# Kernel tuning notes

Hardware: AMD Instinct MI355X
Metric: run time of the kernel (lower is better)

The kernel has to match this reference:

```python
import jax, jax.numpy as jnp
import numpy as np

EPS = 1e-8
THRESHOLD_FACTOR = 0.5


def setup_inputs() -> dict:
    key = jax.random.key(0)
    k1, k2, k3 = jax.random.split(key, 3)
    B, S, D_IN, D_OUT = 4, 4096, 2048, 2048
    x = jax.random.normal(k1, (B, S, D_IN), dtype=jnp.float32)
    # kaiming-uniform-like init for weight
    bound = 1.0 / np.sqrt(D_IN)
    weight = jax.random.uniform(k2, (D_OUT, D_IN), dtype=jnp.float32,
                                minval=-np.sqrt(3.0) * bound, maxval=np.sqrt(3.0) * bound)
    row_scale = jnp.ones((D_OUT, 1), dtype=jnp.float32)
    bias = jax.random.uniform(k3, (D_OUT,), dtype=jnp.float32, minval=-bound, maxval=bound)
    g = jnp.ones((D_IN,), dtype=jnp.float32)  # input RMSNorm affine weight
    return {"x": x, "weight": weight, "row_scale": row_scale, "bias": bias, "g": g}


def _rms_norm(v, axis):
    return v * jax.lax.rsqrt(jnp.mean(v * v, axis=axis, keepdims=True) + EPS)


def reference(x, weight, row_scale, bias, g):
    # input RMSNorm with affine scale
    xn = _rms_norm(x, -1) * g  # [B,S,Din]
    # row RMSNorm of weight
    w = _rms_norm(weight, 1)  # [Dout,Din]
    # abs-mean threshold ternary quantization
    abs_mean = jnp.mean(jnp.abs(w), axis=1, keepdims=True)  # [Dout,1]
    mask = (jnp.abs(w) > THRESHOLD_FACTOR * abs_mean).astype(w.dtype)
    w_q = jnp.sign(w) * mask  # ternary {-1,0,1}
    # scaled dequant: per-row abs_mean and learned row_scale
    w_eff = w_q * abs_mean * row_scale  # [Dout,Din]
    out = jnp.einsum('bsd,od->bso', xn, w_eff) + bias
    return out
```

## Files before the change

### kernel.cpp

```cpp
#include <hip/hip_runtime.h>
#include <stdint.h>

#define EPSF 1e-8f

using i32x4 = __attribute__((ext_vector_type(4))) int;

__device__ __forceinline__ float wave_sum(float v) {
#pragma unroll
  for (int off = 32; off > 0; off >>= 1) v += __shfl_down(v, off, 64);
  return v;
}
__device__ __forceinline__ float wave_max(float v) {
#pragma unroll
  for (int off = 32; off > 0; off >>= 1) v = fmaxf(v, __shfl_down(v, off, 64));
  return v;
}

__global__ __launch_bounds__(256) void wquant_kernel(
    const float* __restrict__ w, const float* __restrict__ row_scale,
    signed char* __restrict__ wq, float* __restrict__ scale, int K) {
  const int row = blockIdx.x;
  const int t = threadIdx.x;
  const float* wr = w + (size_t)row * K;
  float4 v0 = reinterpret_cast<const float4*>(wr)[2 * t];
  float4 v1 = reinterpret_cast<const float4*>(wr)[2 * t + 1];
  float f[8] = {v0.x, v0.y, v0.z, v0.w, v1.x, v1.y, v1.z, v1.w};
  float sa = 0.f, sq = 0.f;
#pragma unroll
  for (int i = 0; i < 8; ++i) { sa += fabsf(f[i]); sq += f[i] * f[i]; }
  sa = wave_sum(sa);
  sq = wave_sum(sq);
  __shared__ float smA[4], smQ[4];
  const int wid = t >> 6;
  if ((t & 63) == 0) { smA[wid] = sa; smQ[wid] = sq; }
  __syncthreads();
  const float sumabs = smA[0] + smA[1] + smA[2] + smA[3];
  const float sumsq  = smQ[0] + smQ[1] + smQ[2] + smQ[3];
  const float absmean = sumabs / (float)K;
  const float thr = 0.5f * absmean;
  union { signed char c[8]; uint2 u; } pk;
#pragma unroll
  for (int i = 0; i < 8; ++i)
    pk.c[i] = (fabsf(f[i]) > thr) ? (f[i] > 0.f ? (signed char)1 : (signed char)-1)
                                  : (signed char)0;
  reinterpret_cast<uint2*>(wq + (size_t)row * K)[t] = pk.u;
  if (t == 0)
    scale[row] = absmean * rsqrtf(sumsq / (float)K + EPSF) * row_scale[row];
}

__global__ __launch_bounds__(256) void xnorm_kernel(
    const float* __restrict__ x, const float* __restrict__ g,
    signed char* __restrict__ xq, float* __restrict__ sx, int K) {
  const int row = blockIdx.x;
  const int t = threadIdx.x;
  const float* xr = x + (size_t)row * K;
  float4 v0 = reinterpret_cast<const float4*>(xr)[2 * t];
  float4 v1 = reinterpret_cast<const float4*>(xr)[2 * t + 1];
  float f[8] = {v0.x, v0.y, v0.z, v0.w, v1.x, v1.y, v1.z, v1.w};
  float sq = 0.f;
#pragma unroll
  for (int i = 0; i < 8; ++i) sq += f[i] * f[i];
  sq = wave_sum(sq);
  __shared__ float smQ[4], smM[4];
  const int wid = t >> 6;
  if ((t & 63) == 0) smQ[wid] = sq;
  __syncthreads();
  const float sumsq = smQ[0] + smQ[1] + smQ[2] + smQ[3];
  const float rs = rsqrtf(sumsq / (float)K + EPSF);
  float4 g0 = reinterpret_cast<const float4*>(g)[2 * t];
  float4 g1 = reinterpret_cast<const float4*>(g)[2 * t + 1];
  float gg[8] = {g0.x, g0.y, g0.z, g0.w, g1.x, g1.y, g1.z, g1.w};
  float vv[8]; float am = 0.f;
#pragma unroll
  for (int i = 0; i < 8; ++i) {
    vv[i] = f[i] * rs * gg[i];
    am = fmaxf(am, fabsf(vv[i]));
  }
  am = wave_max(am);
  if ((t & 63) == 0) smM[wid] = am;
  __syncthreads();
  const float amax = fmaxf(fmaxf(smM[0], smM[1]), fmaxf(smM[2], smM[3]));
  const float inv = amax > 0.f ? 127.f / amax : 0.f;
  union { signed char c[8]; uint2 u; } pk;
#pragma unroll
  for (int i = 0; i < 8; ++i)
    pk.c[i] = (signed char)__float2int_rn(vv[i] * inv);
  reinterpret_cast<uint2*>(xq + (size_t)row * K)[t] = pk.u;
  if (t == 0) sx[row] = amax > 0.f ? amax / 127.f : 0.f;
}


#define BAR() do { __builtin_amdgcn_sched_barrier(0); \
                   asm volatile("" ::: "memory"); \
                   __builtin_amdgcn_s_barrier(); \
                   asm volatile("" ::: "memory"); \
                   __builtin_amdgcn_sched_barrier(0); } while (0)
#define VM(n) asm volatile("s_waitcnt vmcnt(" #n ")" ::: "memory")

__global__ __launch_bounds__(512, 2) void gemm_kernel(
    const signed char* __restrict__ A,
    const signed char* __restrict__ B,
    const float* __restrict__ scale, const float* __restrict__ bias,
    const float* __restrict__ sx,
    float* __restrict__ C, int M, int N, int K) {
  __shared__ signed char lds[2][2][2][16384];

  const int tid  = threadIdx.x;
  const int lane = tid & 63;
  const int wid  = tid >> 6;
  const int wm   = wid >> 2;
  const int wn   = wid & 3;
  const int fr   = lane & 15;
  const int kq   = lane >> 4;

  const int nwg = gridDim.x;
  const int cpx = nwg >> 3;
  const int swz = (blockIdx.x & 7) * cpx + (blockIdx.x >> 3);
  const int NBN = N >> 8;
  const int bn = swz % NBN;
  const int bm = swz / NBN;
  const int mBase = bm * 256, nBase = bn * 256;

  const size_t Kb = (size_t)K;

  const int sr = tid >> 3;
  const int gsrc = (tid & 7) ^ (sr & 7);
  const char* Abyte = (const char*)A + (size_t)(mBase + sr) * Kb + gsrc * 16;
  const char* Bbyte = (const char*)B +
      (size_t)(nBase + ((sr >> 5) * 64) + (sr & 31)) * Kb + gsrc * 16;

#define STAGE_A(bufi, h, t) do { \
    __builtin_amdgcn_global_load_lds( \
      (const __attribute__((address_space(1))) void*)(Abyte + (size_t)((h) * 64) * Kb + (size_t)(t) * 128), \
      (__attribute__((address_space(3))) void*)(&lds[bufi][0][h][tid * 16]), 16, 0, 0); \
    __builtin_amdgcn_global_load_lds( \
      (const __attribute__((address_space(1))) void*)(Abyte + (size_t)(128 + (h) * 64) * Kb + (size_t)(t) * 128), \
      (__attribute__((address_space(3))) void*)(&lds[bufi][0][h][8192 + tid * 16]), 16, 0, 0); \
  } while (0)

#define STAGE_B(bufi, h, t) do { \
    __builtin_amdgcn_global_load_lds( \
      (const __attribute__((address_space(1))) void*)(Bbyte + (size_t)((h) * 32) * Kb + (size_t)(t) * 128), \
      (__attribute__((address_space(3))) void*)(&lds[bufi][1][h][tid * 16]), 16, 0, 0); \
    __builtin_amdgcn_global_load_lds( \
      (const __attribute__((address_space(1))) void*)(Bbyte + (size_t)(128 + (h) * 32) * Kb + (size_t)(t) * 128), \
      (__attribute__((address_space(3))) void*)(&lds[bufi][1][h][8192 + tid * 16]), 16, 0, 0); \
  } while (0)

  const int slot0 = ((kq ^ (fr & 7)) << 4);
  const int aRowB = (wm * 64 + fr) * 128;
  const int bRowB = (wn * 32 + fr) * 128;

  i32x4 aF[4][2], bF[4][2];
  i32x4 acc[8][4];
#pragma unroll
  for (int m = 0; m < 8; ++m)
#pragma unroll
    for (int n = 0; n < 4; ++n) acc[m][n] = (i32x4){0, 0, 0, 0};

#define LDA(bufi, mg) do { \
    _Pragma("unroll") for (int mm = 0; mm < 4; ++mm) \
    _Pragma("unroll") for (int s = 0; s < 2; ++s) \
      aF[mm][s] = *(const i32x4*)&lds[bufi][0][mg][ \
          aRowB + mm * 2048 + (slot0 ^ (s << 6))]; \
  } while (0)

#define LDB(bufi, np) do { \
    _Pragma("unroll") for (int nn = 0; nn < 2; ++nn) \
    _Pragma("unroll") for (int s = 0; s < 2; ++s) \
      bF[(np) * 2 + nn][s] = *(const i32x4*)&lds[bufi][1][np][ \
          bRowB + nn * 2048 + (slot0 ^ (s << 6))]; \
  } while (0)

#define MFMA_Q(mg, np) do { \
    __builtin_amdgcn_s_setprio(1); \
    _Pragma("unroll") for (int mm = 0; mm < 4; ++mm) \
    _Pragma("unroll") for (int nn = 0; nn < 2; ++nn) { \
      i32x4 c = acc[(mg) * 4 + mm][(np) * 2 + nn]; \
      c = __builtin_amdgcn_mfma_i32_16x16x64_i8(aF[mm][0], bF[(np) * 2 + nn][0], c, 0, 0, 0); \
      c = __builtin_amdgcn_mfma_i32_16x16x64_i8(aF[mm][1], bF[(np) * 2 + nn][1], c, 0, 0, 0); \
      acc[(mg) * 4 + mm][(np) * 2 + nn] = c; \
    } \
    __builtin_amdgcn_s_setprio(0); } while (0)

  const int crowBase = mBase + wm * 128 + kq * 4;
  const int ccolBase = nBase + wn * 64 + fr;

#define STORE_Q(mg, np) do { \
    float sxq_[4][4]; \
    _Pragma("unroll") for (int mm = 0; mm < 4; ++mm) \
    _Pragma("unroll") for (int r = 0; r < 4; ++r) \
      sxq_[mm][r] = sx[crowBase + ((mg) * 4 + mm) * 16 + r]; \
    _Pragma("unroll") for (int nn = 0; nn < 2; ++nn) { \
      const int gc = ccolBase + ((np) * 2 + nn) * 16; \
      const float sc = scale[gc]; \
      const float bi = bias[gc]; \
      _Pragma("unroll") for (int mm = 0; mm < 4; ++mm) { \
        const int r0 = crowBase + ((mg) * 4 + mm) * 16; \
        _Pragma("unroll") for (int r = 0; r < 4; ++r) \
          C[(size_t)(r0 + r) * (size_t)N + (size_t)gc] = \
              (float)acc[(mg) * 4 + mm][(np) * 2 + nn][r] * (sxq_[mm][r] * sc) + bi; \
      } } } while (0)

  STAGE_A(0, 0, 0); STAGE_B(0, 0, 0);
  STAGE_A(0, 1, 0); STAGE_B(0, 1, 0);
  STAGE_A(1, 0, 1); STAGE_B(1, 0, 1);
  VM(8);
  BAR();

  const int NT = K >> 7;
  for (int i = 0; i < (NT >> 1) - 1; ++i) {
    const int t1  = 2 * i + 1;
    const int tn0 = 2 * i + 2;
    const int tn1 = 2 * i + 3;
    LDA(0, 0); LDB(0, 0); STAGE_A(1, 1, t1); VM(6);
    BAR(); MFMA_Q(0, 0);
    LDB(0, 1); STAGE_B(1, 1, t1);
    BAR(); MFMA_Q(0, 1);
    LDA(0, 1); STAGE_A(0, 0, tn0);
    BAR(); MFMA_Q(1, 0);
    STAGE_B(0, 0, tn0); VM(8);
    BAR(); MFMA_Q(1, 1);
    LDA(1, 0); LDB(1, 0); STAGE_A(0, 1, tn0); VM(6);
    BAR(); MFMA_Q(0, 0);
    LDB(1, 1); STAGE_B(0, 1, tn0);
    BAR(); MFMA_Q(0, 1);
    LDA(1, 1); STAGE_A(1, 0, tn1);
    BAR(); MFMA_Q(1, 0);
    STAGE_B(1, 0, tn1); VM(8);
    BAR(); MFMA_Q(1, 1);
  }

  {
    const int tl = NT - 1;
    LDA(0, 0); LDB(0, 0); STAGE_A(1, 1, tl); VM(6);
    BAR(); MFMA_Q(0, 0);
    LDB(0, 1); STAGE_B(1, 1, tl);
    BAR(); MFMA_Q(0, 1);
    LDA(0, 1);
    BAR(); MFMA_Q(1, 0);
    VM(4);
    BAR(); MFMA_Q(1, 1);
    LDA(1, 0); LDB(1, 0); VM(0);
    BAR(); MFMA_Q(0, 0); STORE_Q(0, 0);
    LDB(1, 1);
    BAR(); MFMA_Q(0, 1); STORE_Q(0, 1);
    LDA(1, 1);
    BAR(); MFMA_Q(1, 0); STORE_Q(1, 0);
    BAR(); MFMA_Q(1, 1); STORE_Q(1, 1);
  }
#undef STAGE_A
#undef STAGE_B
#undef LDA
#undef LDB
#undef MFMA_Q
#undef STORE_Q
}

extern "C" void kernel_launch(void* const* d_in, const int* in_sizes, int n_in,
                              void* d_out, int out_size, void* d_ws, size_t ws_size,
                              hipStream_t stream) {
  const float* x         = (const float*)d_in[0];
  const float* weight    = (const float*)d_in[1];
  const float* row_scale = (const float*)d_in[2];
  const float* bias      = (const float*)d_in[3];
  const float* g         = (const float*)d_in[4];
  float* out = (float*)d_out;

  const int Din  = in_sizes[4];
  const int Dout = in_sizes[3];
  const int Mrows = in_sizes[0] / Din;

  char* ws = (char*)d_ws;
  signed char* wq = (signed char*)ws;
  signed char* xq = (signed char*)(ws + (size_t)Dout * Din);
  float* scale = (float*)(ws + (size_t)Dout * Din + (size_t)Mrows * Din);
  float* sx = scale + Dout;

  wquant_kernel<<<Dout, 256, 0, stream>>>(weight, row_scale, wq, scale, Din);
  xnorm_kernel<<<Mrows, 256, 0, stream>>>(x, g, xq, sx, Din);
  const int grid = (Mrows / 256) * (Dout / 256);
  gemm_kernel<<<grid, 512, 0, stream>>>(xq, wq, scale, bias, sx, out,
                                        Mrows, Dout, Din);
}
```

Baseline: 114.2 us.

## Switch int8 GEMM inner product to 32x32x32 MFMA tiles

Replaces the 16x16x64 int8 MFMA with the 32x32x32 variant. The LDS fragment loads, accumulator layout and epilogue row/column mapping are reworked to match the new lane layout. Larger MFMA tiles carry more work per instruction and reuse each operand fragment more, which should lower LDS read traffic and instruction-issue overhead. The cost is a new swizzle and store mapping that must line up with the existing staging layout, and strided epilogue writes.

```diff
diff --git a/kernel.cpp b/kernel.cpp
--- a/kernel.cpp
+++ b/kernel.cpp
@@ -3,7 +3,8 @@
 
 #define EPSF 1e-8f
 
-using i32x4 = __attribute__((ext_vector_type(4))) int;
+using i32x4  = __attribute__((ext_vector_type(4))) int;
+using i32x16 = __attribute__((ext_vector_type(16))) int;
 
 __device__ __forceinline__ float wave_sum(float v) {
 #pragma unroll
@@ -110,8 +111,8 @@
   const int wid  = tid >> 6;
   const int wm   = wid >> 2;
   const int wn   = wid & 3;
-  const int fr   = lane & 15;
-  const int kq   = lane >> 4;
+  const int l31  = lane & 31;
+  const int b5   = lane >> 5;
 
   const int nwg = gridDim.x;
   const int cpx = nwg >> 3;
@@ -147,59 +148,56 @@
       (__attribute__((address_space(3))) void*)(&lds[bufi][1][h][8192 + tid * 16]), 16, 0, 0); \
   } while (0)
 
-  const int slot0 = ((kq ^ (fr & 7)) << 4);
-  const int aRowB = (wm * 64 + fr) * 128;
-  const int bRowB = (wn * 32 + fr) * 128;
-
-  i32x4 aF[4][2], bF[4][2];
-  i32x4 acc[8][4];
-#pragma unroll
-  for (int m = 0; m < 8; ++m)
-#pragma unroll
-    for (int n = 0; n < 4; ++n) acc[m][n] = (i32x4){0, 0, 0, 0};
+  const int slotB0 = ((b5 ^ (lane & 7)) << 4);
+  const int aRowB = (wm * 64 + l31) * 128;
+  const int bRowB = (wn * 32 + l31) * 128;
+
+  i32x4 aF[2][4], bF[2][4];
+  i32x16 acc[4][2];
+#pragma unroll
+  for (int m = 0; m < 4; ++m)
+#pragma unroll
+    for (int n = 0; n < 2; ++n)
+#pragma unroll
+      for (int r = 0; r < 16; ++r) acc[m][n][r] = 0;
 
 #define LDA(bufi, mg) do { \
-    _Pragma("unroll") for (int mm = 0; mm < 4; ++mm) \
-    _Pragma("unroll") for (int s = 0; s < 2; ++s) \
-      aF[mm][s] = *(const i32x4*)&lds[bufi][0][mg][ \
-          aRowB + mm * 2048 + (slot0 ^ (s << 6))]; \
+    _Pragma("unroll") for (int mt2 = 0; mt2 < 2; ++mt2) \
+    _Pragma("unroll") for (int s = 0; s < 4; ++s) \
+      aF[mt2][s] = *(const i32x4*)&lds[bufi][0][mg][ \
+          aRowB + mt2 * 4096 + (slotB0 ^ (s << 5))]; \
   } while (0)
 
 #define LDB(bufi, np) do { \
-    _Pragma("unroll") for (int nn = 0; nn < 2; ++nn) \
-    _Pragma("unroll") for (int s = 0; s < 2; ++s) \
-      bF[(np) * 2 + nn][s] = *(const i32x4*)&lds[bufi][1][np][ \
-          bRowB + nn * 2048 + (slot0 ^ (s << 6))]; \
+    _Pragma("unroll") for (int s = 0; s < 4; ++s) \
+      bF[np][s] = *(const i32x4*)&lds[bufi][1][np][ \
+          bRowB + (slotB0 ^ (s << 5))]; \
   } while (0)
 
 #define MFMA_Q(mg, np) do { \
     __builtin_amdgcn_s_setprio(1); \
-    _Pragma("unroll") for (int mm = 0; mm < 4; ++mm) \
-    _Pragma("unroll") for (int nn = 0; nn < 2; ++nn) { \
-      i32x4 c = acc[(mg) * 4 + mm][(np) * 2 + nn]; \
-      c = __builtin_amdgcn_mfma_i32_16x16x64_i8(aF[mm][0], bF[(np) * 2 + nn][0], c, 0, 0, 0); \
-      c = __builtin_amdgcn_mfma_i32_16x16x64_i8(aF[mm][1], bF[(np) * 2 + nn][1], c, 0, 0, 0); \
-      acc[(mg) * 4 + mm][(np) * 2 + nn] = c; \
-    } \
+    _Pragma("unroll") for (int s = 0; s < 4; ++s) \
+    _Pragma("unroll") for (int mt2 = 0; mt2 < 2; ++mt2) \
+      acc[(mg) * 2 + mt2][np] = __builtin_amdgcn_mfma_i32_32x32x32_i8( \
+          aF[mt2][s], bF[np][s], acc[(mg) * 2 + mt2][np], 0, 0, 0); \
     __builtin_amdgcn_s_setprio(0); } while (0)
 
-  const int crowBase = mBase + wm * 128 + kq * 4;
-  const int ccolBase = nBase + wn * 64 + fr;
+  const int crow32 = mBase + wm * 128 + 4 * b5;
+  const int ccol32 = nBase + wn * 64 + l31;
 
 #define STORE_Q(mg, np) do { \
-    float sxq_[4][4]; \
-    _Pragma("unroll") for (int mm = 0; mm < 4; ++mm) \
-    _Pragma("unroll") for (int r = 0; r < 4; ++r) \
-      sxq_[mm][r] = sx[crowBase + ((mg) * 4 + mm) * 16 + r]; \
-    _Pragma("unroll") for (int nn = 0; nn < 2; ++nn) { \
-      const int gc = ccolBase + ((np) * 2 + nn) * 16; \
-      const float sc = scale[gc]; \
-      const float bi = bias[gc]; \
-      _Pragma("unroll") for (int mm = 0; mm < 4; ++mm) { \
-        const int r0 = crowBase + ((mg) * 4 + mm) * 16; \
-        _Pragma("unroll") for (int r = 0; r < 4; ++r) \
-          C[(size_t)(r0 + r) * (size_t)N + (size_t)gc] = \
-              (float)acc[(mg) * 4 + mm][(np) * 2 + nn][r] * (sxq_[mm][r] * sc) + bi; \
+    const int gc = ccol32 + (np) * 32; \
+    const float sc = scale[gc]; \
+    const float bi = bias[gc]; \
+    _Pragma("unroll") for (int mt2 = 0; mt2 < 2; ++mt2) { \
+      const int rb = crow32 + (mg) * 64 + mt2 * 32; \
+      float sxv[16]; \
+      _Pragma("unroll") for (int reg = 0; reg < 16; ++reg) \
+        sxv[reg] = sx[rb + (reg & 3) + 8 * (reg >> 2)]; \
+      _Pragma("unroll") for (int reg = 0; reg < 16; ++reg) { \
+        const int r = rb + (reg & 3) + 8 * (reg >> 2); \
+        C[(size_t)r * (size_t)N + (size_t)gc] = \
+            (float)acc[(mg) * 2 + mt2][np][reg] * (sxv[reg] * sc) + bi; \
       } } } while (0)
 
   STAGE_A(0, 0, 0); STAGE_B(0, 0, 0);
```

Result: slower. 124.1 us (+8.7%).

## Halve barriers per K-tile pair by regrouping staging, LDS reads and MFMAs

Applied to the files above, without the earlier changes.

Reorders the GEMM main loop so each half-tile has two barriers instead of four, issuing both A and B global-to-LDS stages together and grouping MFMA quadrants in pairs. The aim is to cut barrier stalls and the vmcnt waits between MFMA groups. In exchange, each MFMA burst waits longer on LDS reads and there is a risk of LDS buffer hazards if stage/read ordering is wrong.

```diff
diff --git a/kernel.cpp b/kernel.cpp
--- a/kernel.cpp
+++ b/kernel.cpp
@@ -205,49 +205,47 @@
   STAGE_A(0, 0, 0); STAGE_B(0, 0, 0);
   STAGE_A(0, 1, 0); STAGE_B(0, 1, 0);
   STAGE_A(1, 0, 1); STAGE_B(1, 0, 1);
-  VM(8);
-  BAR();
 
   const int NT = K >> 7;
   for (int i = 0; i < (NT >> 1) - 1; ++i) {
     const int t1  = 2 * i + 1;
     const int tn0 = 2 * i + 2;
     const int tn1 = 2 * i + 3;
-    LDA(0, 0); LDB(0, 0); STAGE_A(1, 1, t1); VM(6);
-    BAR(); MFMA_Q(0, 0);
-    LDB(0, 1); STAGE_B(1, 1, t1);
-    BAR(); MFMA_Q(0, 1);
-    LDA(0, 1); STAGE_A(0, 0, tn0);
-    BAR(); MFMA_Q(1, 0);
-    STAGE_B(0, 0, tn0); VM(8);
-    BAR(); MFMA_Q(1, 1);
-    LDA(1, 0); LDB(1, 0); STAGE_A(0, 1, tn0); VM(6);
-    BAR(); MFMA_Q(0, 0);
-    LDB(1, 1); STAGE_B(0, 1, tn0);
-    BAR(); MFMA_Q(0, 1);
-    LDA(1, 1); STAGE_A(1, 0, tn1);
-    BAR(); MFMA_Q(1, 0);
-    STAGE_B(1, 0, tn1); VM(8);
-    BAR(); MFMA_Q(1, 1);
+    VM(4); BAR();
+    STAGE_A(1, 1, t1); STAGE_B(1, 1, t1);
+    LDA(0, 0); LDB(0, 0); LDB(0, 1);
+    MFMA_Q(0, 0); MFMA_Q(0, 1);
+    BAR();
+    STAGE_A(0, 0, tn0); STAGE_B(0, 0, tn0);
+    LDA(0, 1);
+    MFMA_Q(1, 0); MFMA_Q(1, 1);
+    VM(4); BAR();
+    STAGE_A(0, 1, tn0); STAGE_B(0, 1, tn0);
+    LDA(1, 0); LDB(1, 0); LDB(1, 1);
+    MFMA_Q(0, 0); MFMA_Q(0, 1);
+    BAR();
+    STAGE_A(1, 0, tn1); STAGE_B(1, 0, tn1);
+    LDA(1, 1);
+    MFMA_Q(1, 0); MFMA_Q(1, 1);
   }
 
   {
     const int tl = NT - 1;
-    LDA(0, 0); LDB(0, 0); STAGE_A(1, 1, tl); VM(6);
-    BAR(); MFMA_Q(0, 0);
-    LDB(0, 1); STAGE_B(1, 1, tl);
-    BAR(); MFMA_Q(0, 1);
+    VM(4); BAR();
+    STAGE_A(1, 1, tl); STAGE_B(1, 1, tl);
+    LDA(0, 0); LDB(0, 0); LDB(0, 1);
+    MFMA_Q(0, 0); MFMA_Q(0, 1);
+    BAR();
     LDA(0, 1);
-    BAR(); MFMA_Q(1, 0);
-    VM(4);
-    BAR(); MFMA_Q(1, 1);
-    LDA(1, 0); LDB(1, 0); VM(0);
-    BAR(); MFMA_Q(0, 0); STORE_Q(0, 0);
-    LDB(1, 1);
-    BAR(); MFMA_Q(0, 1); STORE_Q(0, 1);
+    MFMA_Q(1, 0); MFMA_Q(1, 1);
+    VM(0); BAR();
+    LDA(1, 0); LDB(1, 0); LDB(1, 1);
+    MFMA_Q(0, 0); STORE_Q(0, 0);
+    MFMA_Q(0, 1); STORE_Q(0, 1);
+    BAR();
     LDA(1, 1);
-    BAR(); MFMA_Q(1, 0); STORE_Q(1, 0);
-    BAR(); MFMA_Q(1, 1); STORE_Q(1, 1);
+    MFMA_Q(1, 0); STORE_Q(1, 0);
+    MFMA_Q(1, 1); STORE_Q(1, 1);
   }
 #undef STAGE_A
 #undef STAGE_B
```

New measurement: 116.4 us. No clear change (+1.9%).

## Fuse prep kernels and compute two N tiles per GEMM block

Applied to the files above, without the earlier changes.

The weight-quantize and activation-normalize kernels are merged into one launch, with blocks split by index, to drop a launch and let both kinds of row work share the device. The GEMM block now computes two adjacent 256-column output tiles in sequence, reusing the A rows. It also prefetches the second tile's operands while the first tile's epilogue stores run. This halves the GEMM grid to one block per CU, which may reduce latency hiding compared with two co-resident blocks per CU.

```diff
diff --git a/kernel.cpp b/kernel.cpp
--- a/kernel.cpp
+++ b/kernel.cpp
@@ -16,77 +16,76 @@
   return v;
 }
 
-__global__ __launch_bounds__(256) void wquant_kernel(
+__global__ __launch_bounds__(256) void prep_kernel(
+    const float* __restrict__ x, const float* __restrict__ g,
     const float* __restrict__ w, const float* __restrict__ row_scale,
-    signed char* __restrict__ wq, float* __restrict__ scale, int K) {
-  const int row = blockIdx.x;
+    signed char* __restrict__ xq, float* __restrict__ sx,
+    signed char* __restrict__ wq, float* __restrict__ scale,
+    int K, int Dout) {
+  __shared__ float smA[4], smQ[4], smM[4];
   const int t = threadIdx.x;
-  const float* wr = w + (size_t)row * K;
-  float4 v0 = reinterpret_cast<const float4*>(wr)[2 * t];
-  float4 v1 = reinterpret_cast<const float4*>(wr)[2 * t + 1];
-  float f[8] = {v0.x, v0.y, v0.z, v0.w, v1.x, v1.y, v1.z, v1.w};
-  float sa = 0.f, sq = 0.f;
-#pragma unroll
-  for (int i = 0; i < 8; ++i) { sa += fabsf(f[i]); sq += f[i] * f[i]; }
-  sa = wave_sum(sa);
-  sq = wave_sum(sq);
-  __shared__ float smA[4], smQ[4];
   const int wid = t >> 6;
-  if ((t & 63) == 0) { smA[wid] = sa; smQ[wid] = sq; }
-  __syncthreads();
-  const float sumabs = smA[0] + smA[1] + smA[2] + smA[3];
-  const float sumsq  = smQ[0] + smQ[1] + smQ[2] + smQ[3];
-  const float absmean = sumabs / (float)K;
-  const float thr = 0.5f * absmean;
-  union { signed char c[8]; uint2 u; } pk;
-#pragma unroll
-  for (int i = 0; i < 8; ++i)
-    pk.c[i] = (fabsf(f[i]) > thr) ? (f[i] > 0.f ? (signed char)1 : (signed char)-1)
-                                  : (signed char)0;
-  reinterpret_cast<uint2*>(wq + (size_t)row * K)[t] = pk.u;
-  if (t == 0)
-    scale[row] = absmean * rsqrtf(sumsq / (float)K + EPSF) * row_scale[row];
-}
-
-__global__ __launch_bounds__(256) void xnorm_kernel(
-    const float* __restrict__ x, const float* __restrict__ g,
-    signed char* __restrict__ xq, float* __restrict__ sx, int K) {
-  const int row = blockIdx.x;
-  const int t = threadIdx.x;
-  const float* xr = x + (size_t)row * K;
-  float4 v0 = reinterpret_cast<const float4*>(xr)[2 * t];
-  float4 v1 = reinterpret_cast<const float4*>(xr)[2 * t + 1];
-  float f[8] = {v0.x, v0.y, v0.z, v0.w, v1.x, v1.y, v1.z, v1.w};
-  float sq = 0.f;
-#pragma unroll
-  for (int i = 0; i < 8; ++i) sq += f[i] * f[i];
-  sq = wave_sum(sq);
-  __shared__ float smQ[4], smM[4];
-  const int wid = t >> 6;
-  if ((t & 63) == 0) smQ[wid] = sq;
-  __syncthreads();
-  const float sumsq = smQ[0] + smQ[1] + smQ[2] + smQ[3];
-  const float rs = rsqrtf(sumsq / (float)K + EPSF);
-  float4 g0 = reinterpret_cast<const float4*>(g)[2 * t];
-  float4 g1 = reinterpret_cast<const float4*>(g)[2 * t + 1];
-  float gg[8] = {g0.x, g0.y, g0.z, g0.w, g1.x, g1.y, g1.z, g1.w};
-  float vv[8]; float am = 0.f;
-#pragma unroll
-  for (int i = 0; i < 8; ++i) {
-    vv[i] = f[i] * rs * gg[i];
-    am = fmaxf(am, fabsf(vv[i]));
-  }
-  am = wave_max(am);
-  if ((t & 63) == 0) smM[wid] = am;
-  __syncthreads();
-  const float amax = fmaxf(fmaxf(smM[0], smM[1]), fmaxf(smM[2], smM[3]));
-  const float inv = amax > 0.f ? 127.f / amax : 0.f;
-  union { signed char c[8]; uint2 u; } pk;
-#pragma unroll
-  for (int i = 0; i < 8; ++i)
-    pk.c[i] = (signed char)__float2int_rn(vv[i] * inv);
-  reinterpret_cast<uint2*>(xq + (size_t)row * K)[t] = pk.u;
-  if (t == 0) sx[row] = amax > 0.f ? amax / 127.f : 0.f;
+  if ((int)blockIdx.x < Dout) {
+    const int row = blockIdx.x;
+    const float* wr = w + (size_t)row * K;
+    float4 v0 = reinterpret_cast<const float4*>(wr)[2 * t];
+    float4 v1 = reinterpret_cast<const float4*>(wr)[2 * t + 1];
+    float f[8] = {v0.x, v0.y, v0.z, v0.w, v1.x, v1.y, v1.z, v1.w};
+    float sa = 0.f, sq = 0.f;
+#pragma unroll
+    for (int i = 0; i < 8; ++i) { sa += fabsf(f[i]); sq += f[i] * f[i]; }
+    sa = wave_sum(sa);
+    sq = wave_sum(sq);
+    if ((t & 63) == 0) { smA[wid] = sa; smQ[wid] = sq; }
+    __syncthreads();
+    const float sumabs = smA[0] + smA[1] + smA[2] + smA[3];
+    const float sumsq  = smQ[0] + smQ[1] + smQ[2] + smQ[3];
+    const float absmean = sumabs / (float)K;
+    const float thr = 0.5f * absmean;
+    union { signed char c[8]; uint2 u; } pk;
+#pragma unroll
+    for (int i = 0; i < 8; ++i)
+      pk.c[i] = (fabsf(f[i]) > thr)
+                    ? (f[i] > 0.f ? (signed char)1 : (signed char)-1)
+                    : (signed char)0;
+    reinterpret_cast<uint2*>(wq + (size_t)row * K)[t] = pk.u;
+    if (t == 0)
+      scale[row] = absmean * rsqrtf(sumsq / (float)K + EPSF) * row_scale[row];
+  } else {
+    const int row = blockIdx.x - Dout;
+    const float* xr = x + (size_t)row * K;
+    float4 v0 = reinterpret_cast<const float4*>(xr)[2 * t];
+    float4 v1 = reinterpret_cast<const float4*>(xr)[2 * t + 1];
+    float f[8] = {v0.x, v0.y, v0.z, v0.w, v1.x, v1.y, v1.z, v1.w};
+    float sq = 0.f;
+#pragma unroll
+    for (int i = 0; i < 8; ++i) sq += f[i] * f[i];
+    sq = wave_sum(sq);
+    if ((t & 63) == 0) smQ[wid] = sq;
+    __syncthreads();
+    const float sumsq = smQ[0] + smQ[1] + smQ[2] + smQ[3];
+    const float rs = rsqrtf(sumsq / (float)K + EPSF);
+    float4 g0 = reinterpret_cast<const float4*>(g)[2 * t];
+    float4 g1 = reinterpret_cast<const float4*>(g)[2 * t + 1];
+    float gg[8] = {g0.x, g0.y, g0.z, g0.w, g1.x, g1.y, g1.z, g1.w};
+    float vv[8]; float am = 0.f;
+#pragma unroll
+    for (int i = 0; i < 8; ++i) {
+      vv[i] = f[i] * rs * gg[i];
+      am = fmaxf(am, fabsf(vv[i]));
+    }
+    am = wave_max(am);
+    if ((t & 63) == 0) smM[wid] = am;
+    __syncthreads();
+    const float amax = fmaxf(fmaxf(smM[0], smM[1]), fmaxf(smM[2], smM[3]));
+    const float inv = amax > 0.f ? 127.f / amax : 0.f;
+    union { signed char c[8]; uint2 u; } pk;
+#pragma unroll
+    for (int i = 0; i < 8; ++i)
+      pk.c[i] = (signed char)__float2int_rn(vv[i] * inv);
+    reinterpret_cast<uint2*>(xq + (size_t)row * K)[t] = pk.u;
+    if (t == 0) sx[row] = amax > 0.f ? amax / 127.f : 0.f;
+  }
 }
 
 
@@ -116,10 +115,12 @@
   const int nwg = gridDim.x;
   const int cpx = nwg >> 3;
   const int swz = (blockIdx.x & 7) * cpx + (blockIdx.x >> 3);
-  const int NBN = N >> 8;
-  const int bn = swz % NBN;
-  const int bm = swz / NBN;
-  const int mBase = bm * 256, nBase = bn * 256;
+  const int NBP = N >> 9;
+  const int bp = swz % NBP;
+  const int bm = swz / NBP;
+  const int mBase = bm * 256;
+  const int nBase1 = bp * 512;
+  const int nBase2 = nBase1 + 256;
 
   const size_t Kb = (size_t)K;
 
@@ -127,7 +128,8 @@
   const int gsrc = (tid & 7) ^ (sr & 7);
   const char* Abyte = (const char*)A + (size_t)(mBase + sr) * Kb + gsrc * 16;
   const char* Bbyte = (const char*)B +
-      (size_t)(nBase + ((sr >> 5) * 64) + (sr & 31)) * Kb + gsrc * 16;
+      (size_t)(nBase1 + ((sr >> 5) * 64) + (sr & 31)) * Kb + gsrc * 16;
+  const size_t bOff2 = (size_t)256 * Kb;
 
 #define STAGE_A(bufi, h, t) do { \
     __builtin_amdgcn_global_load_lds( \
@@ -138,12 +140,12 @@
       (__attribute__((address_space(3))) void*)(&lds[bufi][0][h][8192 + tid * 16]), 16, 0, 0); \
   } while (0)
 
-#define STAGE_B(bufi, h, t) do { \
+#define STAGE_B(bufi, h, t, bo) do { \
     __builtin_amdgcn_global_load_lds( \
-      (const __attribute__((address_space(1))) void*)(Bbyte + (size_t)((h) * 32) * Kb + (size_t)(t) * 128), \
+      (const __attribute__((address_space(1))) void*)(Bbyte + (bo) + (size_t)((h) * 32) * Kb + (size_t)(t) * 128), \
       (__attribute__((address_space(3))) void*)(&lds[bufi][1][h][tid * 16]), 16, 0, 0); \
     __builtin_amdgcn_global_load_lds( \
-      (const __attribute__((address_space(1))) void*)(Bbyte + (size_t)(128 + (h) * 32) * Kb + (size_t)(t) * 128), \
+      (const __attribute__((address_space(1))) void*)(Bbyte + (bo) + (size_t)(128 + (h) * 32) * Kb + (size_t)(t) * 128), \
       (__attribute__((address_space(3))) void*)(&lds[bufi][1][h][8192 + tid * 16]), 16, 0, 0); \
   } while (0)
 
@@ -184,15 +186,14 @@
     __builtin_amdgcn_s_setprio(0); } while (0)
 
   const int crowBase = mBase + wm * 128 + kq * 4;
-  const int ccolBase = nBase + wn * 64 + fr;
-
-#define STORE_Q(mg, np) do { \
+
+#define STORE_Q(mg, np, cb) do { \
     float sxq_[4][4]; \
     _Pragma("unroll") for (int mm = 0; mm < 4; ++mm) \
     _Pragma("unroll") for (int r = 0; r < 4; ++r) \
       sxq_[mm][r] = sx[crowBase + ((mg) * 4 + mm) * 16 + r]; \
     _Pragma("unroll") for (int nn = 0; nn < 2; ++nn) { \
-      const int gc = ccolBase + ((np) * 2 + nn) * 16; \
+      const int gc = (cb) + ((np) * 2 + nn) * 16; \
       const float sc = scale[gc]; \
       const float bi = bias[gc]; \
       _Pragma("unroll") for (int mm = 0; mm < 4; ++mm) { \
@@ -202,32 +203,35 @@
               (float)acc[(mg) * 4 + mm][(np) * 2 + nn][r] * (sxq_[mm][r] * sc) + bi; \
       } } } while (0)
 
-  STAGE_A(0, 0, 0); STAGE_B(0, 0, 0);
-  STAGE_A(0, 1, 0); STAGE_B(0, 1, 0);
-  STAGE_A(1, 0, 1); STAGE_B(1, 0, 1);
+  const int ccol1 = nBase1 + wn * 64 + fr;
+  const int ccol2 = nBase2 + wn * 64 + fr;
+  const int NT = K >> 7;
+
+  STAGE_A(0, 0, 0); STAGE_B(0, 0, 0, 0);
+  STAGE_A(0, 1, 0); STAGE_B(0, 1, 0, 0);
+  STAGE_A(1, 0, 1); STAGE_B(1, 0, 1, 0);
   VM(8);
   BAR();
 
-  const int NT = K >> 7;
   for (int i = 0; i < (NT >> 1) - 1; ++i) {
     const int t1  = 2 * i + 1;
     const int tn0 = 2 * i + 2;
     const int tn1 = 2 * i + 3;
     LDA(0, 0); LDB(0, 0); STAGE_A(1, 1, t1); VM(6);
     BAR(); MFMA_Q(0, 0);
-    LDB(0, 1); STAGE_B(1, 1, t1);
+    LDB(0, 1); STAGE_B(1, 1, t1, 0);
     BAR(); MFMA_Q(0, 1);
     LDA(0, 1); STAGE_A(0, 0, tn0);
     BAR(); MFMA_Q(1, 0);
-    STAGE_B(0, 0, tn0); VM(8);
+    STAGE_B(0, 0, tn0, 0); VM(8);
     BAR(); MFMA_Q(1, 1);
     LDA(1, 0); LDB(1, 0); STAGE_A(0, 1, tn0); VM(6);
     BAR(); MFMA_Q(0, 0);
-    LDB(1, 1); STAGE_B(0, 1, tn0);
+    LDB(1, 1); STAGE_B(0, 1, tn0, 0);
     BAR(); MFMA_Q(0, 1);
     LDA(1, 1); STAGE_A(1, 0, tn1);
     BAR(); MFMA_Q(1, 0);
-    STAGE_B(1, 0, tn1); VM(8);
+    STAGE_B(1, 0, tn1, 0); VM(8);
     BAR(); MFMA_Q(1, 1);
   }
 
@@ -235,19 +239,70 @@
     const int tl = NT - 1;
     LDA(0, 0); LDB(0, 0); STAGE_A(1, 1, tl); VM(6);
     BAR(); MFMA_Q(0, 0);
-    LDB(0, 1); STAGE_B(1, 1, tl);
+    LDB(0, 1); STAGE_B(1, 1, tl, 0);
     BAR(); MFMA_Q(0, 1);
     LDA(0, 1);
     BAR(); MFMA_Q(1, 0);
     VM(4);
     BAR(); MFMA_Q(1, 1);
+    LDA(1, 0); LDB(1, 0);
+    STAGE_A(0, 0, 0); STAGE_B(0, 0, 0, bOff2);
+    VM(4);
+    BAR(); MFMA_Q(0, 0); STORE_Q(0, 0, ccol1);
+    LDB(1, 1); STAGE_A(0, 1, 0);
+    BAR(); MFMA_Q(0, 1); STORE_Q(0, 1, ccol1);
+    LDA(1, 1); STAGE_B(0, 1, 0, bOff2);
+    BAR(); MFMA_Q(1, 0); STORE_Q(1, 0, ccol1);
+    STAGE_A(1, 0, 1);
+    BAR(); MFMA_Q(1, 1); STORE_Q(1, 1, ccol1);
+    STAGE_B(1, 0, 1, bOff2);
+    VM(8);
+#pragma unroll
+    for (int m = 0; m < 8; ++m)
+#pragma unroll
+      for (int n = 0; n < 4; ++n) acc[m][n] = (i32x4){0, 0, 0, 0};
+    BAR();
+  }
+
+  for (int i = 0; i < (NT >> 1) - 1; ++i) {
+    const int t1  = 2 * i + 1;
+    const int tn0 = 2 * i + 2;
+    const int tn1 = 2 * i + 3;
+    LDA(0, 0); LDB(0, 0); STAGE_A(1, 1, t1); VM(6);
+    BAR(); MFMA_Q(0, 0);
+    LDB(0, 1); STAGE_B(1, 1, t1, bOff2);
+    BAR(); MFMA_Q(0, 1);
+    LDA(0, 1); STAGE_A(0, 0, tn0);
+    BAR(); MFMA_Q(1, 0);
+    STAGE_B(0, 0, tn0, bOff2); VM(8);
+    BAR(); MFMA_Q(1, 1);
+    LDA(1, 0); LDB(1, 0); STAGE_A(0, 1, tn0); VM(6);
+    BAR(); MFMA_Q(0, 0);
+    LDB(1, 1); STAGE_B(0, 1, tn0, bOff2);
+    BAR(); MFMA_Q(0, 1);
+    LDA(1, 1); STAGE_A(1, 0, tn1);
+    BAR(); MFMA_Q(1, 0);
+    STAGE_B(1, 0, tn1, bOff2); VM(8);
+    BAR(); MFMA_Q(1, 1);
+  }
+
+  {
+    const int tl = NT - 1;
+    LDA(0, 0); LDB(0, 0); STAGE_A(1, 1, tl); VM(6);
+    BAR(); MFMA_Q(0, 0);
+    LDB(0, 1); STAGE_B(1, 1, tl, bOff2);
+    BAR(); MFMA_Q(0, 1);
+    LDA(0, 1);
+    BAR(); MFMA_Q(1, 0);
+    VM(4);
+    BAR(); MFMA_Q(1, 1);
     LDA(1, 0); LDB(1, 0); VM(0);
-    BAR(); MFMA_Q(0, 0); STORE_Q(0, 0);
+    BAR(); MFMA_Q(0, 0); STORE_Q(0, 0, ccol2);
     LDB(1, 1);
-    BAR(); MFMA_Q(0, 1); STORE_Q(0, 1);
+    BAR(); MFMA_Q(0, 1); STORE_Q(0, 1, ccol2);
     LDA(1, 1);
-    BAR(); MFMA_Q(1, 0); STORE_Q(1, 0);
-    BAR(); MFMA_Q(1, 1); STORE_Q(1, 1);
+    BAR(); MFMA_Q(1, 0); STORE_Q(1, 0, ccol2);
+    BAR(); MFMA_Q(1, 1); STORE_Q(1, 1, ccol2);
   }
 #undef STAGE_A
 #undef STAGE_B
@@ -277,9 +332,9 @@
   float* scale = (float*)(ws + (size_t)Dout * Din + (size_t)Mrows * Din);
   float* sx = scale + Dout;
 
-  wquant_kernel<<<Dout, 256, 0, stream>>>(weight, row_scale, wq, scale, Din);
-  xnorm_kernel<<<Mrows, 256, 0, stream>>>(x, g, xq, sx, Din);
-  const int grid = (Mrows / 256) * (Dout / 256);
+  prep_kernel<<<Dout + Mrows, 256, 0, stream>>>(x, g, weight, row_scale,
+                                                xq, sx, wq, scale, Din, Dout);
+  const int grid = (Mrows / 256) * (Dout / 512);
   gemm_kernel<<<grid, 512, 0, stream>>>(xq, wq, scale, bias, sx, out,
                                         Mrows, Dout, Din);
 }
```

Measured after the change: 133.9 us. +17.2%, slower.
